# Kernel optimization log

Measured on AMD Instinct MI355X. Metric: run time of the kernel, lower is better.

The kernel has to match this reference:

```python
import jax, jax.numpy as jnp
import numpy as np

N, E = 10000, 320000
F_N, F_E, F_G, LATENT, F_OUT = 128, 128, 32, 128, 128


def _make_mlp_params(key, dims):
    # dims: list of layer widths, e.g. [256,128,128,128,256]
    params = []
    for i in range(len(dims) - 1):
        key, k1, k2 = jax.random.split(key, 3)
        lim = 1.0 / np.sqrt(dims[i])
        w = jax.random.uniform(k1, (dims[i], dims[i + 1]), jnp.float32, -lim, lim)
        b = jax.random.uniform(k2, (dims[i + 1],), jnp.float32, -lim, lim)
        params.append((w, b))
    return params, key


def _mlp(h, ws, bs, activate_final):
    n = len(ws)
    for i in range(n):
        h = h @ ws[i] + bs[i]
        if i < n - 1 or activate_final:
            h = jax.nn.relu(h)
    return h


def setup_inputs() -> dict:
    key = jax.random.key(0)
    key, kx, ke, kg, ki = jax.random.split(key, 5)
    x = jax.random.normal(kx, (N, F_N), jnp.float32)
    edge_index = jax.random.randint(ki, (2, E), 0, N, jnp.int64)
    edge_attr = jax.random.normal(ke, (E, F_E), jnp.float32)
    global_attr = jax.random.normal(kg, (1, F_G), jnp.float32)

    # node_mlp_1: (F_N+F_E) -> L -> L -> L -> (F_N+F_E), activate_final=True
    p1, key = _make_mlp_params(key, [F_N + F_E, LATENT, LATENT, LATENT, F_N + F_E])
    # node_mlp_2: (2*F_N+F_E+F_G) -> L -> L -> L -> F_OUT, activate_final=False
    p2, key = _make_mlp_params(key, [2 * F_N + F_E + F_G, LATENT, LATENT, LATENT, F_OUT])

    inp = {"x": x, "edge_index": edge_index, "edge_attr": edge_attr, "global_attr": global_attr}
    for i, (w, b) in enumerate(p1):
        inp[f"m1_w{i}"] = w
        inp[f"m1_b{i}"] = b
    for i, (w, b) in enumerate(p2):
        inp[f"m2_w{i}"] = w
        inp[f"m2_b{i}"] = b
    return inp


def reference(x, edge_index, edge_attr, global_attr,
              m1_w0, m1_b0, m1_w1, m1_b1, m1_w2, m1_b2, m1_w3, m1_b3,
              m2_w0, m2_b0, m2_w1, m2_b1, m2_w2, m2_b2, m2_w3, m2_b3):
    row, col = edge_index[0], edge_index[1]
    n = x.shape[0]
    # gather sender-side node feats, per-edge MLP (activate_final=True)
    h = jnp.concatenate([x[row], edge_attr], axis=1)          # [E, F_N+F_E]
    h = _mlp(h, [m1_w0, m1_w1, m1_w2, m1_w3], [m1_b0, m1_b1, m1_b2, m1_b3], True)
    # scatter_mean over destination nodes
    s = jax.ops.segment_sum(h, col, num_segments=n)           # [N, F_N+F_E]
    cnt = jax.ops.segment_sum(jnp.ones((h.shape[0],), h.dtype), col, num_segments=n)
    agg = s / jnp.maximum(cnt, 1.0)[:, None]
    # repeat global feats to N rows (pad_to_size mode='repeat', G divides N)
    g = jnp.tile(global_attr, (n // global_attr.shape[0], 1))  # [N, F_G]
    out = jnp.concatenate([x, agg, g], axis=1)                 # [N, 2F_N+F_E+F_G]
    return _mlp(out, [m2_w0, m2_w1, m2_w2, m2_w3], [m2_b0, m2_b1, m2_b2, m2_b3], False)
```

## Files before the change

### kernel.cpp

```cpp
#include <hip/hip_runtime.h>
#include <hip/hip_bf16.h>

#define E_EDGES 320000
#define N_NODES 10000

typedef __attribute__((ext_vector_type(8))) short short8;
typedef __attribute__((ext_vector_type(4))) float floatx4;

__device__ __forceinline__ float bf2f(unsigned short u) {
    union { unsigned int i; float f; } v; v.i = ((unsigned int)u) << 16; return v.f;
}
__device__ __forceinline__ unsigned int pk2(float a, float b) {
    float2 t; t.x = a; t.y = b;
    __hip_bfloat162 h = __float22bfloat162_rn(t);
    union { __hip_bfloat162 h; unsigned int u; } c; c.h = h; return c.u;
}

template<int K, int Nn, int ET, bool BDB>
__device__ __forceinline__ void layer_pre(const unsigned short* __restrict__ in, int istride,
                                          const unsigned short* __restrict__ wt,
                                          int lane, int n0, floatx4 (&acc)[2][ET])
{
    constexpr int KT = K / 32;
    const int quad = lane >> 4;
    const int mrow = lane & 15;

    short8 a[KT][2];
#pragma unroll
    for (int kt = 0; kt < KT; ++kt)
#pragma unroll
        for (int ft = 0; ft < 2; ++ft)
            a[kt][ft] = *(const short8*)&wt[(size_t)(kt * (Nn >> 4) + (n0 >> 4) + ft) * 512 + lane * 8];

    floatx4 zero = {0.f, 0.f, 0.f, 0.f};
#pragma unroll
    for (int ft = 0; ft < 2; ++ft)
#pragma unroll
        for (int et = 0; et < ET; ++et)
            acc[ft][et] = zero;

    if constexpr (BDB) {
        short8 b[2][ET];
#pragma unroll
        for (int et = 0; et < ET; ++et)
            b[0][et] = *(const short8*)&in[(et * 16 + mrow) * istride + quad * 8];
#pragma unroll
        for (int kt = 0; kt < KT; ++kt) {
            if (kt + 1 < KT) {
                const int koff = (kt + 1) * 32 + quad * 8;
#pragma unroll
                for (int et = 0; et < ET; ++et)
                    b[(kt + 1) & 1][et] = *(const short8*)&in[(et * 16 + mrow) * istride + koff];
            }
#pragma unroll
            for (int ft = 0; ft < 2; ++ft)
#pragma unroll
                for (int et = 0; et < ET; ++et)
                    acc[ft][et] = __builtin_amdgcn_mfma_f32_16x16x32_bf16(a[kt][ft], b[kt & 1][et], acc[ft][et], 0, 0, 0);
        }
    } else {
#pragma unroll
        for (int kt = 0; kt < KT; ++kt) {
            const int koff = kt * 32 + quad * 8;
            short8 b[ET];
#pragma unroll
            for (int et = 0; et < ET; ++et)
                b[et] = *(const short8*)&in[(et * 16 + mrow) * istride + koff];
#pragma unroll
            for (int ft = 0; ft < 2; ++ft)
#pragma unroll
                for (int et = 0; et < ET; ++et)
                    acc[ft][et] = __builtin_amdgcn_mfma_f32_16x16x32_bf16(a[kt][ft], b[et], acc[ft][et], 0, 0, 0);
        }
    }
}

template<int K, int Nn, int ET>
__device__ __forceinline__ void layer_stream(const unsigned short* __restrict__ in, int istride,
                                             const unsigned short* __restrict__ wt,
                                             int lane, int n0, floatx4 (&acc)[2][ET])
{
    constexpr int KT = K / 32;
    const int quad = lane >> 4;
    const int mrow = lane & 15;

    floatx4 zero = {0.f, 0.f, 0.f, 0.f};
#pragma unroll
    for (int ft = 0; ft < 2; ++ft)
#pragma unroll
        for (int et = 0; et < ET; ++et)
            acc[ft][et] = zero;

    short8 a[2][2];
    short8 b[2][ET];
#pragma unroll
    for (int ft = 0; ft < 2; ++ft)
        a[0][ft] = *(const short8*)&wt[(size_t)((n0 >> 4) + ft) * 512 + lane * 8];
#pragma unroll
    for (int et = 0; et < ET; ++et)
        b[0][et] = *(const short8*)&in[(et * 16 + mrow) * istride + quad * 8];

#pragma unroll
    for (int kt = 0; kt < KT; ++kt) {
        if (kt + 1 < KT) {
            const int nb = (kt + 1) & 1;
            const int koff = (kt + 1) * 32 + quad * 8;
#pragma unroll
            for (int ft = 0; ft < 2; ++ft)
                a[nb][ft] = *(const short8*)&wt[(size_t)((kt + 1) * (Nn >> 4) + (n0 >> 4) + ft) * 512 + lane * 8];
#pragma unroll
            for (int et = 0; et < ET; ++et)
                b[nb][et] = *(const short8*)&in[(et * 16 + mrow) * istride + koff];
        }
#pragma unroll
        for (int ft = 0; ft < 2; ++ft)
#pragma unroll
            for (int et = 0; et < ET; ++et)
                acc[ft][et] = __builtin_amdgcn_mfma_f32_16x16x32_bf16(a[kt & 1][ft], b[kt & 1][et], acc[ft][et], 0, 0, 0);
    }
}

template<int FT, int ET>
__device__ __forceinline__ void store_lds(floatx4 (&acc)[FT][ET], const float* __restrict__ bias,
                                          int lane, int n0, unsigned short* __restrict__ out, int ostride,
                                          bool relu)
{
    const int quad = lane >> 4, mrow = lane & 15;
#pragma unroll
    for (int ft = 0; ft < FT; ++ft) {
        int fbase = n0 + ft * 16 + quad * 4;
        float4 bv = *(const float4*)&bias[fbase];
#pragma unroll
        for (int et = 0; et < ET; ++et) {
            int edge = et * 16 + mrow;
            float v0 = acc[ft][et][0] + bv.x;
            float v1 = acc[ft][et][1] + bv.y;
            float v2 = acc[ft][et][2] + bv.z;
            float v3 = acc[ft][et][3] + bv.w;
            if (relu) {
                v0 = v0 > 0.f ? v0 : 0.f; v1 = v1 > 0.f ? v1 : 0.f;
                v2 = v2 > 0.f ? v2 : 0.f; v3 = v3 > 0.f ? v3 : 0.f;
            }
            uint2 pk; pk.x = pk2(v0, v1); pk.y = pk2(v2, v3);
            *(uint2*)&out[edge * ostride + fbase] = pk;
        }
    }
}

struct TDesc { const float* src; unsigned short* dst; int nElem; int logN; int blockStart; };
struct TArgs { TDesc d[8]; };

__global__ void prep_kernel(TArgs a, const int* __restrict__ eidx, int* __restrict__ cnt, int histStart)
{
    int b = blockIdx.x;
    if (b >= histStart) {
        int e = (b - histStart) * 256 + threadIdx.x;
        if (e < E_EDGES) atomicAdd(&cnt[eidx[E_EDGES + e]], 1);
        return;
    }
    int i = 0;
#pragma unroll
    for (int j = 1; j < 8; ++j)
        if (b >= a.d[j].blockStart) i = j;
    const TDesc t = a.d[i];
    int idx = (b - t.blockStart) * 256 + threadIdx.x;
    if (idx < t.nElem) {
        int n = idx & ((1 << t.logN) - 1);
        int k = idx >> t.logN;
        int ntiles = 1 << (t.logN - 4);
        size_t dsti = ((size_t)(k >> 5) * ntiles + (n >> 4)) * 512
                    + ((k >> 3) & 3) * 128 + (n & 15) * 8 + (k & 7);
        union { float f; unsigned int u; } c; c.f = t.src[idx];
        unsigned int uu = c.u;
        t.dst[dsti] = (unsigned short)((uu + 0x7fffu + ((uu >> 16) & 1u)) >> 16);
    }
}

__global__ void scan_kernel(const int* __restrict__ cnt, int* __restrict__ fill)
{
    __shared__ int partial[256];
    const int CH = 40;
    int tid = threadIdx.x;
    int base = tid * CH;
    int local[CH];
    int sum = 0;
#pragma unroll
    for (int j = 0; j < CH; ++j) {
        int idx = base + j;
        int c = (idx < N_NODES) ? cnt[idx] : 0;
        local[j] = c;
        sum += c;
    }
    partial[tid] = sum;
    __syncthreads();
    for (int o = 1; o < 256; o <<= 1) {
        int v = (tid >= o) ? partial[tid - o] : 0;
        __syncthreads();
        partial[tid] += v;
        __syncthreads();
    }
    int run = partial[tid] - sum;
#pragma unroll
    for (int j = 0; j < CH; ++j) {
        int idx = base + j;
        if (idx < N_NODES) fill[idx] = run;
        run += local[j];
    }
}

__global__ void fill_kernel(const int* __restrict__ eidx, int* __restrict__ fill,
                            int* __restrict__ elist, int* __restrict__ rowp, int* __restrict__ dstp)
{
    int e = blockIdx.x * 256 + threadIdx.x;
    int c = eidx[E_EDGES + e];
    int r = eidx[e];
    int pos = atomicAdd(&fill[c], 1);
    elist[pos] = e;
    rowp[pos] = r;
    dstp[pos] = c;
}

__global__ __launch_bounds__(256, 3) void edge_kernel(
    const float* __restrict__ x,
    const float* __restrict__ ea,
    const int* __restrict__ elist, const int* __restrict__ rowp, const int* __restrict__ dstp,
    const unsigned short* __restrict__ wt0, const float* __restrict__ b0,
    const unsigned short* __restrict__ wt1, const float* __restrict__ b1,
    const unsigned short* __restrict__ wt2, const float* __restrict__ b2,
    const unsigned short* __restrict__ wt3, const float* __restrict__ b3,
    float* __restrict__ s)
{
    __shared__ __align__(16) char U[51200];
    __shared__ int es[64];
    __shared__ int rs[64];
    __shared__ int ds[64];

    unsigned short* H0 = (unsigned short*)U;
    unsigned short* H1 = (unsigned short*)(U + 33792);
    unsigned short* H2 = (unsigned short*)U;
    unsigned short* H3 = H1;
    unsigned short* G  = (unsigned short*)U;

    const int tid = threadIdx.x;
    const int p0 = blockIdx.x * 64;

    if (tid < 64) {
        es[tid] = elist[p0 + tid];
        rs[tid] = rowp[p0 + tid];
        ds[tid] = dstp[p0 + tid];
    }
    __syncthreads();

#pragma unroll
    for (int i = 0; i < 16; ++i) {
        int task = tid + i * 256;
        int row = task >> 6, part = task & 63;
        float4 v;
        if (part < 32) v = *(const float4*)(x + (size_t)rs[row] * 128 + part * 4);
        else           v = *(const float4*)(ea + (size_t)es[row] * 128 + (part - 32) * 4);
        uint2 pk; pk.x = pk2(v.x, v.y); pk.y = pk2(v.z, v.w);
        *(uint2*)&H0[row * 264 + part * 4] = pk;
    }
    __syncthreads();

    const int lane = tid & 63;
    const int wave = tid >> 6;

    {
        floatx4 acc[2][4];
        layer_pre<256, 128, 4, false>(H0, 264, wt0, lane, wave * 32, acc);
        store_lds<2, 4>(acc, b0, lane, wave * 32, H1, 136, true);
    }
    __syncthreads();
    {
        floatx4 acc[2][4];
        layer_pre<128, 128, 4, true>(H1, 136, wt1, lane, wave * 32, acc);
        store_lds<2, 4>(acc, b1, lane, wave * 32, H2, 136, true);
    }
    __syncthreads();
    {
        floatx4 acc[2][4];
        layer_pre<128, 128, 4, true>(H2, 136, wt2, lane, wave * 32, acc);
        store_lds<2, 4>(acc, b2, lane, wave * 32, H3, 136, true);
    }
    __syncthreads();
    {
        floatx4 acc[2][4];
        layer_pre<128, 256, 4, true>(H3, 136, wt3, lane, wave * 64, acc);
        store_lds<2, 4>(acc, b3, lane, wave * 64, G, 264, true);
        floatx4 acc2[2][4];
        layer_pre<128, 256, 4, true>(H3, 136, wt3, lane, wave * 64 + 32, acc2);
        store_lds<2, 4>(acc2, b3, lane, wave * 64 + 32, G, 264, true);
    }
    __syncthreads();

    {
        int p = tid & 127;
        int half = tid >> 7;
        int col2 = p * 2;
        int base = half * 32;
        float s0 = 0.f, s1 = 0.f;
#pragma unroll 4
        for (int i = 0; i < 32; ++i) {
            int gi = base + i;
            unsigned int u = *(const unsigned int*)&G[gi * 264 + col2];
            s0 += bf2f((unsigned short)u);
            s1 += bf2f((unsigned short)(u >> 16));
            if (i == 31 || ds[gi + 1] != ds[gi]) {
                float* dst = &s[(size_t)ds[gi] * 256 + col2];
                atomicAdd(dst, s0);
                atomicAdd(dst + 1, s1);
                s0 = 0.f; s1 = 0.f;
            }
        }
    }
}

__global__ __launch_bounds__(256, 4) void node_kernel(
    const float* __restrict__ x,
    const float* __restrict__ g,
    const float* __restrict__ s,
    const int* __restrict__ cnt,
    const unsigned short* __restrict__ wt0, const float* __restrict__ b0,
    const unsigned short* __restrict__ wt1, const float* __restrict__ b1,
    const unsigned short* __restrict__ wt2, const float* __restrict__ b2,
    const unsigned short* __restrict__ wt3, const float* __restrict__ b3,
    float* __restrict__ out)
{
    __shared__ __align__(16) char NU[35840];
    unsigned short* Abig = (unsigned short*)NU;
    unsigned short* HsA  = (unsigned short*)(NU + 27136);
    unsigned short* HsB  = (unsigned short*)NU;

    const int tid = threadIdx.x;
    const int node0 = blockIdx.x * 32;

#pragma unroll
    for (int i = 0; i < 4; ++i) {
        int task = tid + i * 256;
        int row = task >> 5, part = task & 31;
        int node = node0 + row;
        uint2 pk = {0u, 0u};
        if (node < N_NODES) {
            float4 v = *(const float4*)(x + (size_t)node * 128 + part * 4);
            pk.x = pk2(v.x, v.y); pk.y = pk2(v.z, v.w);
        }
        *(uint2*)&Abig[row * 424 + part * 4] = pk;
    }
#pragma unroll
    for (int i = 0; i < 8; ++i) {
        int task = tid + i * 256;
        int row = task >> 6, part = task & 63;
        int node = node0 + row;
        uint2 pk = {0u, 0u};
        if (node < N_NODES) {
            float c = (float)cnt[node];
            float inv = 1.f / (c > 1.f ? c : 1.f);
            floatx4 v = *(const floatx4*)(s + (size_t)node * 256 + part * 4);
            pk.x = pk2(v[0] * inv, v[1] * inv);
            pk.y = pk2(v[2] * inv, v[3] * inv);
        }
        *(uint2*)&Abig[row * 424 + 128 + part * 4] = pk;
    }
    {
        int task = tid;
        int row = task >> 3, part = task & 7;
        float4 v = *(const float4*)(g + part * 4);
        uint2 pk; pk.x = pk2(v.x, v.y); pk.y = pk2(v.z, v.w);
        *(uint2*)&Abig[row * 424 + 384 + part * 4] = pk;
    }
    __syncthreads();

    const int lane = tid & 63;
    const int wave = tid >> 6;

    {
        floatx4 acc[2][2];
        layer_stream<416, 128, 2>(Abig, 424, wt0, lane, wave * 32, acc);
        store_lds<2, 2>(acc, b0, lane, wave * 32, HsA, 136, true);
    }
    __syncthreads();
    {
        floatx4 acc[2][2];
        layer_pre<128, 128, 2, true>(HsA, 136, wt1, lane, wave * 32, acc);
        store_lds<2, 2>(acc, b1, lane, wave * 32, HsB, 136, true);
    }
    __syncthreads();
    {
        floatx4 acc[2][2];
        layer_pre<128, 128, 2, true>(HsB, 136, wt2, lane, wave * 32, acc);
        store_lds<2, 2>(acc, b2, lane, wave * 32, HsA, 136, true);
    }
    __syncthreads();
    {
        floatx4 acc[2][2];
        layer_pre<128, 128, 2, true>(HsA, 136, wt3, lane, wave * 32, acc);
        const int quad = lane >> 4, mrow = lane & 15;
#pragma unroll
        for (int ft = 0; ft < 2; ++ft) {
            int fbase = wave * 32 + ft * 16 + quad * 4;
            float4 bv = *(const float4*)&b3[fbase];
#pragma unroll
            for (int et = 0; et < 2; ++et) {
                int node = node0 + et * 16 + mrow;
                if (node < N_NODES) {
                    float4 o;
                    o.x = acc[ft][et][0] + bv.x;
                    o.y = acc[ft][et][1] + bv.y;
                    o.z = acc[ft][et][2] + bv.z;
                    o.w = acc[ft][et][3] + bv.w;
                    *(float4*)&out[(size_t)node * 128 + fbase] = o;
                }
            }
        }
    }
}

extern "C" void kernel_launch(void* const* d_in, const int* in_sizes, int n_in,
                              void* d_out, int out_size, void* d_ws, size_t ws_size,
                              hipStream_t stream)
{
    (void)in_sizes; (void)n_in; (void)out_size; (void)ws_size;

    const float* x  = (const float*)d_in[0];
    const int* eidx = (const int*)d_in[1];
    const float* ea = (const float*)d_in[2];
    const float* g  = (const float*)d_in[3];

    const float* w1[4]  = { (const float*)d_in[4],  (const float*)d_in[6],
                            (const float*)d_in[8],  (const float*)d_in[10] };
    const float* bb1[4] = { (const float*)d_in[5],  (const float*)d_in[7],
                            (const float*)d_in[9],  (const float*)d_in[11] };
    const float* w2[4]  = { (const float*)d_in[12], (const float*)d_in[14],
                            (const float*)d_in[16], (const float*)d_in[18] };
    const float* bb2[4] = { (const float*)d_in[13], (const float*)d_in[15],
                            (const float*)d_in[17], (const float*)d_in[19] };

    char* p = (char*)d_ws;
    unsigned short* wt1_0 = (unsigned short*)p; p += 256 * 128 * 2;
    unsigned short* wt1_1 = (unsigned short*)p; p += 128 * 128 * 2;
    unsigned short* wt1_2 = (unsigned short*)p; p += 128 * 128 * 2;
    unsigned short* wt1_3 = (unsigned short*)p; p += 128 * 256 * 2;
    unsigned short* wt2_0 = (unsigned short*)p; p += 416 * 128 * 2;
    unsigned short* wt2_1 = (unsigned short*)p; p += 128 * 128 * 2;
    unsigned short* wt2_2 = (unsigned short*)p; p += 128 * 128 * 2;
    unsigned short* wt2_3 = (unsigned short*)p; p += 128 * 128 * 2;
    float* s   = (float*)p; p += (size_t)N_NODES * 256 * 4;
    int* cnt   = (int*)p;   p += (size_t)N_NODES * 4;
    int* fill  = (int*)p;   p += (size_t)N_NODES * 4;
    int* elist = (int*)p;   p += (size_t)E_EDGES * 4;
    int* rowp  = (int*)p;   p += (size_t)E_EDGES * 4;
    int* dstp  = (int*)p;   p += (size_t)E_EDGES * 4;

    hipMemsetAsync(s, 0, (size_t)N_NODES * 256 * 4 + (size_t)N_NODES * 4, stream);

    TArgs ta;
    int bs = 0;
    auto set = [&](int i, const float* src, unsigned short* dst, int K, int Nn, int logN) {
        ta.d[i].src = src; ta.d[i].dst = dst; ta.d[i].nElem = K * Nn;
        ta.d[i].logN = logN; ta.d[i].blockStart = bs;
        bs += (K * Nn + 255) / 256;
    };
    set(0, w1[0], wt1_0, 256, 128, 7);
    set(1, w1[1], wt1_1, 128, 128, 7);
    set(2, w1[2], wt1_2, 128, 128, 7);
    set(3, w1[3], wt1_3, 128, 256, 8);
    set(4, w2[0], wt2_0, 416, 128, 7);
    set(5, w2[1], wt2_1, 128, 128, 7);
    set(6, w2[2], wt2_2, 128, 128, 7);
    set(7, w2[3], wt2_3, 128, 128, 7);

    int histBlocks = E_EDGES / 256;
    hipLaunchKernelGGL(prep_kernel, dim3(bs + histBlocks), dim3(256), 0, stream,
                       ta, eidx, cnt, bs);
    hipLaunchKernelGGL(scan_kernel, dim3(1), dim3(256), 0, stream, cnt, fill);
    hipLaunchKernelGGL(fill_kernel, dim3(E_EDGES / 256), dim3(256), 0, stream,
                       eidx, fill, elist, rowp, dstp);

    hipLaunchKernelGGL(edge_kernel, dim3(E_EDGES / 64), dim3(256), 0, stream,
                       x, ea, elist, rowp, dstp,
                       wt1_0, bb1[0], wt1_1, bb1[1], wt1_2, bb1[2], wt1_3, bb1[3],
                       s);

    hipLaunchKernelGGL(node_kernel, dim3((N_NODES + 31) / 32), dim3(256), 0, stream,
                       x, g, s, cnt,
                       wt2_0, bb2[0], wt2_1, bb2[1], wt2_2, bb2[2], wt2_3, bb2[3],
                       (float*)d_out);
}
```

Measured before the change: 477.1 us.

## Prefetch next-layer weights across barriers and pack edge indices into int4

Weight fragments for each MLP layer are now loaded into registers one stage ahead, so their latency overlaps the previous layer's MFMA work. The edge gather loads are issued all at once before conversion, with the first layer's weights fetched in between. The last edge layer now computes all 64 output features in one pass. The three sorted index arrays are merged into one int4 array, making each index fetch a single 16-byte access. The cost is higher register pressure under launch_bounds(256,3), which could cause spills or lower occupancy.

```diff
diff --git a/kernel.cpp b/kernel.cpp
--- a/kernel.cpp
+++ b/kernel.cpp
@@ -16,62 +16,44 @@
     union { __hip_bfloat162 h; unsigned int u; } c; c.h = h; return c.u;
 }
 
-template<int K, int Nn, int ET, bool BDB>
-__device__ __forceinline__ void layer_pre(const unsigned short* __restrict__ in, int istride,
-                                          const unsigned short* __restrict__ wt,
-                                          int lane, int n0, floatx4 (&acc)[2][ET])
+template<int KT, int FT>
+__device__ __forceinline__ void load_a(const unsigned short* __restrict__ wt, int ntiles, int t0,
+                                       int lane, short8 (&a)[KT][FT])
+{
+#pragma unroll
+    for (int kt = 0; kt < KT; ++kt)
+#pragma unroll
+        for (int ft = 0; ft < FT; ++ft)
+            a[kt][ft] = *(const short8*)&wt[(size_t)(kt * ntiles + t0 + ft) * 512 + lane * 8];
+}
+
+template<int K, int FT, int ET>
+__device__ __forceinline__ void layer_mfma(const unsigned short* __restrict__ in, int istride,
+                                           int lane, const short8 (&a)[K / 32][FT],
+                                           floatx4 (&acc)[FT][ET])
 {
     constexpr int KT = K / 32;
     const int quad = lane >> 4;
     const int mrow = lane & 15;
-
-    short8 a[KT][2];
-#pragma unroll
-    for (int kt = 0; kt < KT; ++kt)
-#pragma unroll
-        for (int ft = 0; ft < 2; ++ft)
-            a[kt][ft] = *(const short8*)&wt[(size_t)(kt * (Nn >> 4) + (n0 >> 4) + ft) * 512 + lane * 8];
-
     floatx4 zero = {0.f, 0.f, 0.f, 0.f};
 #pragma unroll
-    for (int ft = 0; ft < 2; ++ft)
+    for (int ft = 0; ft < FT; ++ft)
 #pragma unroll
         for (int et = 0; et < ET; ++et)
             acc[ft][et] = zero;
 
-    if constexpr (BDB) {
-        short8 b[2][ET];
+#pragma unroll
+    for (int kt = 0; kt < KT; ++kt) {
+        const int koff = kt * 32 + quad * 8;
+        short8 b[ET];
 #pragma unroll
         for (int et = 0; et < ET; ++et)
-            b[0][et] = *(const short8*)&in[(et * 16 + mrow) * istride + quad * 8];
-#pragma unroll
-        for (int kt = 0; kt < KT; ++kt) {
-            if (kt + 1 < KT) {
-                const int koff = (kt + 1) * 32 + quad * 8;
-#pragma unroll
-                for (int et = 0; et < ET; ++et)
-                    b[(kt + 1) & 1][et] = *(const short8*)&in[(et * 16 + mrow) * istride + koff];
-            }
-#pragma unroll
-            for (int ft = 0; ft < 2; ++ft)
-#pragma unroll
-                for (int et = 0; et < ET; ++et)
-                    acc[ft][et] = __builtin_amdgcn_mfma_f32_16x16x32_bf16(a[kt][ft], b[kt & 1][et], acc[ft][et], 0, 0, 0);
-        }
-    } else {
-#pragma unroll
-        for (int kt = 0; kt < KT; ++kt) {
-            const int koff = kt * 32 + quad * 8;
-            short8 b[ET];
+            b[et] = *(const short8*)&in[(et * 16 + mrow) * istride + koff];
+#pragma unroll
+        for (int ft = 0; ft < FT; ++ft)
 #pragma unroll
             for (int et = 0; et < ET; ++et)
-                b[et] = *(const short8*)&in[(et * 16 + mrow) * istride + koff];
-#pragma unroll
-            for (int ft = 0; ft < 2; ++ft)
-#pragma unroll
-                for (int et = 0; et < ET; ++et)
-                    acc[ft][et] = __builtin_amdgcn_mfma_f32_16x16x32_bf16(a[kt][ft], b[et], acc[ft][et], 0, 0, 0);
-        }
+                acc[ft][et] = __builtin_amdgcn_mfma_f32_16x16x32_bf16(a[kt][ft], b[et], acc[ft][et], 0, 0, 0);
     }
 }
 
@@ -209,21 +191,19 @@
 }
 
 __global__ void fill_kernel(const int* __restrict__ eidx, int* __restrict__ fill,
-                            int* __restrict__ elist, int* __restrict__ rowp, int* __restrict__ dstp)
+                            int4* __restrict__ pack)
 {
     int e = blockIdx.x * 256 + threadIdx.x;
     int c = eidx[E_EDGES + e];
     int r = eidx[e];
     int pos = atomicAdd(&fill[c], 1);
-    elist[pos] = e;
-    rowp[pos] = r;
-    dstp[pos] = c;
+    pack[pos] = make_int4(e, r, c, 0);
 }
 
 __global__ __launch_bounds__(256, 3) void edge_kernel(
     const float* __restrict__ x,
     const float* __restrict__ ea,
-    const int* __restrict__ elist, const int* __restrict__ rowp, const int* __restrict__ dstp,
+    const int4* __restrict__ pack,
     const unsigned short* __restrict__ wt0, const float* __restrict__ b0,
     const unsigned short* __restrict__ wt1, const float* __restrict__ b1,
     const unsigned short* __restrict__ wt2, const float* __restrict__ b2,
@@ -245,52 +225,71 @@
     const int p0 = blockIdx.x * 64;
 
     if (tid < 64) {
-        es[tid] = elist[p0 + tid];
-        rs[tid] = rowp[p0 + tid];
-        ds[tid] = dstp[p0 + tid];
-    }
-    __syncthreads();
-
+        int4 pr = pack[p0 + tid];
+        es[tid] = pr.x; rs[tid] = pr.y; ds[tid] = pr.z;
+    }
+    __syncthreads();
+
+    const int lane = tid & 63;
+    const int wave = tid >> 6;
+    const int t32 = (wave * 32) >> 4;
+
+    float4 v[16];
 #pragma unroll
     for (int i = 0; i < 16; ++i) {
         int task = tid + i * 256;
         int row = task >> 6, part = task & 63;
-        float4 v;
-        if (part < 32) v = *(const float4*)(x + (size_t)rs[row] * 128 + part * 4);
-        else           v = *(const float4*)(ea + (size_t)es[row] * 128 + (part - 32) * 4);
-        uint2 pk; pk.x = pk2(v.x, v.y); pk.y = pk2(v.z, v.w);
+        const float* src = (part < 32) ? (x  + (size_t)rs[row] * 128 + part * 4)
+                                       : (ea + (size_t)es[row] * 128 + (part - 32) * 4);
+        v[i] = *(const float4*)src;
+    }
+    __builtin_amdgcn_sched_barrier(0);
+    short8 a0[8][2];
+    load_a<8, 2>(wt0, 8, t32, lane, a0);
+    __builtin_amdgcn_sched_barrier(0);
+#pragma unroll
+    for (int i = 0; i < 16; ++i) {
+        int task = tid + i * 256;
+        int row = task >> 6, part = task & 63;
+        uint2 pk; pk.x = pk2(v[i].x, v[i].y); pk.y = pk2(v[i].z, v[i].w);
         *(uint2*)&H0[row * 264 + part * 4] = pk;
     }
     __syncthreads();
 
-    const int lane = tid & 63;
-    const int wave = tid >> 6;
-
+    short8 a1[4][2];
+    load_a<4, 2>(wt1, 8, t32, lane, a1);
+    __builtin_amdgcn_sched_barrier(0);
     {
         floatx4 acc[2][4];
-        layer_pre<256, 128, 4, false>(H0, 264, wt0, lane, wave * 32, acc);
+        layer_mfma<256, 2, 4>(H0, 264, lane, a0, acc);
         store_lds<2, 4>(acc, b0, lane, wave * 32, H1, 136, true);
     }
     __syncthreads();
+
+    short8 a2[4][2];
+    load_a<4, 2>(wt2, 8, t32, lane, a2);
+    __builtin_amdgcn_sched_barrier(0);
     {
         floatx4 acc[2][4];
-        layer_pre<128, 128, 4, true>(H1, 136, wt1, lane, wave * 32, acc);
+        layer_mfma<128, 2, 4>(H1, 136, lane, a1, acc);
         store_lds<2, 4>(acc, b1, lane, wave * 32, H2, 136, true);
     }
     __syncthreads();
+
+    short8 a3[4][4];
+    load_a<4, 4>(wt3, 16, wave * 4, lane, a3);
+    __builtin_amdgcn_sched_barrier(0);
     {
         floatx4 acc[2][4];
-        layer_pre<128, 128, 4, true>(H2, 136, wt2, lane, wave * 32, acc);
+        layer_mfma<128, 2, 4>(H2, 136, lane, a2, acc);
         store_lds<2, 4>(acc, b2, lane, wave * 32, H3, 136, true);
     }
     __syncthreads();
-    {
-        floatx4 acc[2][4];
-        layer_pre<128, 256, 4, true>(H3, 136, wt3, lane, wave * 64, acc);
-        store_lds<2, 4>(acc, b3, lane, wave * 64, G, 264, true);
-        floatx4 acc2[2][4];
-        layer_pre<128, 256, 4, true>(H3, 136, wt3, lane, wave * 64 + 32, acc2);
-        store_lds<2, 4>(acc2, b3, lane, wave * 64 + 32, G, 264, true);
+
+    {
+        floatx4 acc[4][4];
+        layer_mfma<128, 4, 4>(H3, 136, lane, a3, acc);
+        store_lds<4, 4>(acc, b3, lane, wave * 64, G, 264, true);
     }
     __syncthreads();
 
@@ -373,28 +372,41 @@
 
     const int lane = tid & 63;
     const int wave = tid >> 6;
-
+    const int t32 = (wave * 32) >> 4;
+
+    short8 a1[4][2];
+    load_a<4, 2>(wt1, 8, t32, lane, a1);
+    __builtin_amdgcn_sched_barrier(0);
     {
         floatx4 acc[2][2];
         layer_stream<416, 128, 2>(Abig, 424, wt0, lane, wave * 32, acc);
         store_lds<2, 2>(acc, b0, lane, wave * 32, HsA, 136, true);
     }
     __syncthreads();
+
+    short8 a2[4][2];
+    load_a<4, 2>(wt2, 8, t32, lane, a2);
+    __builtin_amdgcn_sched_barrier(0);
     {
         floatx4 acc[2][2];
-        layer_pre<128, 128, 2, true>(HsA, 136, wt1, lane, wave * 32, acc);
+        layer_mfma<128, 2, 2>(HsA, 136, lane, a1, acc);
         store_lds<2, 2>(acc, b1, lane, wave * 32, HsB, 136, true);
     }
     __syncthreads();
+
+    short8 a3[4][2];
+    load_a<4, 2>(wt3, 8, t32, lane, a3);
+    __builtin_amdgcn_sched_barrier(0);
     {
         floatx4 acc[2][2];
-        layer_pre<128, 128, 2, true>(HsB, 136, wt2, lane, wave * 32, acc);
+        layer_mfma<128, 2, 2>(HsB, 136, lane, a2, acc);
         store_lds<2, 2>(acc, b2, lane, wave * 32, HsA, 136, true);
     }
     __syncthreads();
+
     {
         floatx4 acc[2][2];
-        layer_pre<128, 128, 2, true>(HsA, 136, wt3, lane, wave * 32, acc);
+        layer_mfma<128, 2, 2>(HsA, 136, lane, a3, acc);
         const int quad = lane >> 4, mrow = lane & 15;
 #pragma unroll
         for (int ft = 0; ft < 2; ++ft) {
@@ -445,12 +457,10 @@
     unsigned short* wt2_1 = (unsigned short*)p; p += 128 * 128 * 2;
     unsigned short* wt2_2 = (unsigned short*)p; p += 128 * 128 * 2;
     unsigned short* wt2_3 = (unsigned short*)p; p += 128 * 128 * 2;
-    float* s   = (float*)p; p += (size_t)N_NODES * 256 * 4;
-    int* cnt   = (int*)p;   p += (size_t)N_NODES * 4;
-    int* fill  = (int*)p;   p += (size_t)N_NODES * 4;
-    int* elist = (int*)p;   p += (size_t)E_EDGES * 4;
-    int* rowp  = (int*)p;   p += (size_t)E_EDGES * 4;
-    int* dstp  = (int*)p;   p += (size_t)E_EDGES * 4;
+    float* s    = (float*)p; p += (size_t)N_NODES * 256 * 4;
+    int* cnt    = (int*)p;   p += (size_t)N_NODES * 4;
+    int* fill   = (int*)p;   p += (size_t)N_NODES * 4;
+    int4* pack  = (int4*)p;  p += (size_t)E_EDGES * 16;
 
     hipMemsetAsync(s, 0, (size_t)N_NODES * 256 * 4 + (size_t)N_NODES * 4, stream);
 
@@ -475,10 +485,10 @@
                        ta, eidx, cnt, bs);
     hipLaunchKernelGGL(scan_kernel, dim3(1), dim3(256), 0, stream, cnt, fill);
     hipLaunchKernelGGL(fill_kernel, dim3(E_EDGES / 256), dim3(256), 0, stream,
-                       eidx, fill, elist, rowp, dstp);
+                       eidx, fill, pack);
 
     hipLaunchKernelGGL(edge_kernel, dim3(E_EDGES / 64), dim3(256), 0, stream,
-                       x, ea, elist, rowp, dstp,
+                       x, ea, pack,
                        wt1_0, bb1[0], wt1_1, bb1[1], wt1_2, bb1[2], wt1_3, bb1[3],
                        s);
 
```

Result: faster. 405.7 us (-15.0%).
